# Kernel tuning notes

Hardware: AMD Instinct MI355X
Metric: run time of the kernel (lower is better)

Reference implementation:

```python
import jax, jax.numpy as jnp
import numpy as np

# ---- hyperparameters (from pars / init_kwargs) ----
ALPHA = 0.9          # synaptic conductance decay (snn.Synaptic alpha)
BETA = 0.8           # membrane decay (snn.Synaptic beta)
BETA_PLUS = 0.9      # pre-synaptic trace decay
BETA_MINUS = 0.9     # post-synaptic trace decay
THRESHOLD = 1.0
W_MIN, W_MAX = 0.0, 1.0
A_PLUS, A_MINUS = 0.008, 0.0008
T, B, IN, N = 350, 128, 784, 400
SPIKE_P = 0.05       # Bernoulli firing probability of the rate-coded input


def setup_inputs() -> dict:
    key = jax.random.key(0)
    k_img, k_w = jax.random.split(key)
    # Poisson/Bernoulli rate-coded MNIST spike train [T, B, IN]
    image = (jax.random.uniform(k_img, (T, B, IN)) < SPIKE_P).astype(jnp.float32)
    # nn.Linear default init U(-1/sqrt(IN), 1/sqrt(IN)) then clamp to [w_min, w_max]
    s = 1.0 / np.sqrt(IN)
    W = jnp.clip(jax.random.uniform(k_w, (N, IN), minval=-s, maxval=s), W_MIN, W_MAX)
    return {"image": image, "W": W}


def reference(image, W):
    """Fused LIF (snntorch Synaptic, reset-by-subtraction) + STDP loop over T steps.

    Returns (W_final, mem_final, syn_final, total_spikes_per_neuron).
    """
    batch = image.shape[1]

    def step(carry, x_t):
        syn, mem, pre_tr, post_tr, W = carry
        # pre-synaptic trace: tr_t = beta_plus * tr_{t-1} + x_t
        pre_tr = BETA_PLUS * pre_tr + x_t                      # [B, IN]
        # linear projection (no bias)
        I_t = jnp.einsum('bi,ni->bn', x_t, W)                  # [B, N]
        # snntorch Synaptic: reset from pre-update mem, subtract mechanism
        reset = (mem > THRESHOLD).astype(mem.dtype)
        syn = ALPHA * syn + I_t
        mem = BETA * mem + syn - reset * THRESHOLD
        spk = (mem > THRESHOLD).astype(mem.dtype)              # [B, N]
        # post-synaptic trace
        post_tr = BETA_MINUS * post_tr + spk
        # STDP: potentiate on post spike x pre trace, depress on pre spike x post trace
        dW = (A_PLUS * jnp.einsum('bn,bi->ni', spk, pre_tr)
              - A_MINUS * jnp.einsum('bn,bi->ni', post_tr, x_t)) / batch
        W = jnp.clip(W + dW, W_MIN, W_MAX)
        return (syn, mem, pre_tr, post_tr, W), spk.sum(axis=0)

    syn0 = jnp.zeros((batch, N), image.dtype)
    mem0 = jnp.zeros((batch, N), image.dtype)
    pre0 = jnp.zeros((batch, IN), image.dtype)
    post0 = jnp.zeros((batch, N), image.dtype)

    (syn, mem, _, _, W_final), spk_counts = jax.lax.scan(
        step, (syn0, mem0, pre0, post0, W), image)
    return W_final, mem, syn, spk_counts.sum(axis=0)
```

## Files before the change

kernel.cpp:

```cpp
#include <hip/hip_runtime.h>
#include <hip/hip_bf16.h>


#define TT    350
#define BB    128
#define INF   784
#define NNEU  400
#define NS    2
#define NTHR  1024
#define LCAP  80

#define ALPHA 0.9f
#define BETA  0.8f
#define BPLUS 0.9f
#define BMIN  0.9f
#define CP    (0.008f/128.0f)
#define CM    (0.0008f/128.0f)

__device__ __forceinline__ float bf2f(__hip_bfloat16 v){ return __bfloat162float(v); }

__device__ __forceinline__ void barx(){
  asm volatile("s_waitcnt lgkmcnt(0)" ::: "memory");
  __builtin_amdgcn_s_barrier();
  __builtin_amdgcn_sched_barrier(0);
}

__global__ void k_pretr(const float* __restrict__ img, __hip_bfloat16* __restrict__ pre){
  int idx = blockIdx.x*blockDim.x + threadIdx.x;
  if (idx >= BB*INF) return;
  float v = 0.f;
  for (int t=0;t<TT;t++){
    v = BPLUS*v + img[(size_t)t*(BB*INF) + idx];
    pre[(size_t)t*(BB*INF) + idx] = __float2bfloat16(v);
  }
}

__global__ void k_S(const __hip_bfloat16* __restrict__ pre, float* __restrict__ S){
  int idx = blockIdx.x*blockDim.x + threadIdx.x;
  if (idx >= TT*INF) return;
  int t = idx / INF, i = idx - t*INF;
  const __hip_bfloat16* p = pre + (size_t)t*(BB*INF) + i;
  float s = 0.f;
  for (int b=0;b<BB;b++) s += bf2f(p[(size_t)b*INF]);
  S[idx] = s;
}

__global__ void k_masks(const float* __restrict__ img,
                        unsigned short* __restrict__ lists,
                        int* __restrict__ cnts,
                        unsigned int* __restrict__ collist){
  __shared__ unsigned long long rowbits[BB][13];
  __shared__ unsigned short buf[16][LCAP];
  const int t = blockIdx.x;
  const int tid = threadIdx.x, lane = tid & 63, w = tid >> 6;
  const float* base = img + (size_t)t*(BB*INF);

  for (int r8=0; r8<8; r8++){
    int r = w*8 + r8;
    const float* p = base + (size_t)r*INF;
    for (int c=0;c<13;c++){
      int i = c*64 + lane;
      bool a = (i < INF) && (p[i] > 0.f);
      unsigned long long bal = __ballot(a);
      if (lane == 0) rowbits[r][c] = bal;
    }
  }
  for (int r8=0; r8<8; r8++){
    int r = w*8 + r8;
    int cnt = 0;
    for (int c=0;c<13;c++){
      unsigned long long word = rowbits[r][c];
      int i = c*64 + lane;
      bool a = (word >> lane) & 1ull;
      int pos = cnt + __popcll(word & ((1ull<<lane)-1ull));
      if (a && pos < LCAP) buf[w][pos] = (unsigned short)(i<<3);
      cnt += __popcll(word);
    }
    for (int k = cnt + lane; k < LCAP; k += 64) buf[w][k] = (unsigned short)(INF<<3);
    if (lane == 0) cnts[t*BB + r] = (cnt < LCAP) ? cnt : LCAP;
    if (lane < LCAP/2)
      ((unsigned int*)(lists + (size_t)(t*BB + r)*LCAP))[lane] = ((unsigned int*)buf[w])[lane];
  }
  __syncthreads();
  if (tid < INF){
    int wsel = tid >> 6, bit = tid & 63;
    unsigned long long m0=0, m1=0;
    for (int b=0;b<64;b++) m0 |= ((rowbits[b][wsel]    >> bit) & 1ull) << b;
    for (int b=0;b<64;b++) m1 |= ((rowbits[64+b][wsel] >> bit) & 1ull) << b;
    int cnt = __popcll(m0) + __popcll(m1);
    unsigned int wd[8];
    wd[0] = (unsigned int)cnt; wd[1]=0;wd[2]=0;wd[3]=0;wd[4]=0;wd[5]=0;wd[6]=0;wd[7]=0;
    #pragma unroll
    for (int k=1;k<32;k++){
      int bb;
      if (m0){ bb = __builtin_ctzll(m0); m0 &= m0-1; }
      else if (m1){ bb = 64 + __builtin_ctzll(m1); m1 &= m1-1; }
      else bb = 128;
      wd[k>>2] |= ((unsigned int)bb) << ((k&3)*8);
    }
    uint4* dst = (uint4*)(collist + ((size_t)t*INF + tid)*8);
    uint4 lo; lo.x=wd[0]; lo.y=wd[1]; lo.z=wd[2]; lo.w=wd[3];
    uint4 hi; hi.x=wd[4]; hi.y=wd[5]; hi.z=wd[6]; hi.w=wd[7];
    dst[0]=lo; dst[1]=hi;
  }
}

__device__ __forceinline__ float potf(unsigned long long ma, unsigned long long mb,
                                      int pc, float Sv,
                                      const __hip_bfloat16* __restrict__ prt, int c){
  bool direct = (pc <= 64);
  unsigned long long m = direct ? ma : ~ma;
  unsigned long long n = direct ? mb : ~mb;
  float acc = 0.f;
  while (m){ int bb = __builtin_ctzll(m); m &= m-1; acc += bf2f(prt[(size_t)bb*INF + c]); }
  while (n){ int bb = __builtin_ctzll(n); n &= n-1; acc += bf2f(prt[(size_t)(64+bb)*INF + c]); }
  return direct ? acc : (Sv - acc);
}

#define G2(W) { float2 a_ = *(const float2*)((const char*)&Wp2[0] + ((W) & 0xffffu)); I0 += a_.x; I1 += a_.y; \
                float2 b_ = *(const float2*)((const char*)&Wp2[0] + ((W) >> 16));     I0 += b_.x; I1 += b_.y; }
#define GATHER8(V) { G2((V).x); G2((V).y); G2((V).z); G2((V).w); }

#define DEP4(W) { float2 p_; \
  p_ = postl[(W) & 0xffu];        d0 += p_.x; d1 += p_.y; \
  p_ = postl[((W)>>8) & 0xffu];   d0 += p_.x; d1 += p_.y; \
  p_ = postl[((W)>>16) & 0xffu];  d0 += p_.x; d1 += p_.y; \
  p_ = postl[(W)>>24];            d0 += p_.x; d1 += p_.y; }

#define DOCOL(c, cl, sv) { \
  float d0=0.f, d1=0.f; \
  unsigned int w0_ = (cl).x; \
  { float2 p_; \
    p_ = postl[(w0_>>8) & 0xffu];  d0 += p_.x; d1 += p_.y; \
    p_ = postl[(w0_>>16) & 0xffu]; d0 += p_.x; d1 += p_.y; \
    p_ = postl[w0_>>24];           d0 += p_.x; d1 += p_.y; } \
  DEP4((cl).y); DEP4((cl).z); DEP4((cl).w); \
  int cc_ = (int)(w0_ & 0xffu); \
  if (cc_ > 15){ \
    uint4 e2_ = *(const uint4*)(collist + ((size_t)t*INF + (c))*8 + 4); \
    DEP4(e2_.x); DEP4(e2_.y); DEP4(e2_.z); DEP4(e2_.w); \
  } \
  float pot0_ = potf(s00, s01, pc0, (sv), prt, (c)); \
  float pot1_ = potf(s10, s11, pc1, (sv), prt, (c)); \
  float2 wv_ = Wp2[(c)]; \
  wv_.x = fminf(fmaxf(wv_.x + CP*pot0_ - CM*d0, 0.f), 1.f); \
  wv_.y = fminf(fmaxf(wv_.y + CP*pot1_ - CM*d1, 0.f), 1.f); \
  Wp2[(c)] = wv_; }

__launch_bounds__(NTHR, 1)
__global__ void k_main(const float* __restrict__ Win,
                       const __hip_bfloat16* __restrict__ pre,
                       const float* __restrict__ S,
                       const unsigned short* __restrict__ lists,
                       const int* __restrict__ cnts,
                       const unsigned int* __restrict__ collist,
                       float* __restrict__ out){
  __shared__ float2 Wp2[800];
  __shared__ float2 postl[132];
  __shared__ unsigned long long smQ[2][2];
  __shared__ float cntS[2];
  __shared__ float2 postCb[2];
  __shared__ int    unifb[2];

  const int tid  = threadIdx.x;
  const int lane = tid & 63;
  const int wv   = tid >> 6;
  const int q    = lane >> 3;
  const int b    = (wv << 3) | (lane & 7);
  const int n0   = blockIdx.x * NS;

  if (tid < 800){
    float2 w;
    w.x = (tid < INF) ? Win[(size_t)n0*INF + tid] : 0.f;
    w.y = (tid < INF) ? Win[(size_t)(n0+1)*INF + tid] : 0.f;
    Wp2[tid] = w;
  }
  if (tid < 132){ postl[tid].x = 0.f; postl[tid].y = 0.f; }
  if (tid < 2) cntS[tid] = 0.f;
  if (tid == 0){
    postCb[0].x = 0.f; postCb[0].y = 0.f; unifb[0] = 1;
    postCb[1].x = 0.f; postCb[1].y = 0.f; unifb[1] = 1;
  }

  const int  c0   = tid;
  const bool hasc = (c0 < INF);

  float syn0=0.f, mem0=0.f, syn1=0.f, mem1=0.f, sc0=0.f, sc1=0.f;

  uint4 lA = *(const uint4*)(lists + ((size_t)b)*LCAP + (size_t)q*8);
  int cn = cnts[b];
  uint4 cl0; cl0.x=0;cl0.y=0;cl0.z=0;cl0.w=0;
  float sv0 = 0.f;
  if (hasc){ cl0 = *(const uint4*)(collist + (size_t)c0*8); sv0 = S[c0]; }

  __syncthreads();

  for (int t=0; t<TT; t++){
    float I0 = 0.f, I1 = 0.f;
    GATHER8(lA);
    if (cn > 64 + q*8){
      uint4 lC = *(const uint4*)(lists + ((size_t)t*BB + b)*LCAP + 64 + (size_t)q*8);
      GATHER8(lC);
    }
    int tn = (t+1 < TT) ? t+1 : TT-1;
    uint4 lAn = *(const uint4*)(lists + ((size_t)tn*BB + b)*LCAP + (size_t)q*8);
    int cnn = cnts[tn*BB + b];
    uint4 cl0n = cl0; float sv0n = sv0;
    if (hasc){
      cl0n = *(const uint4*)(collist + ((size_t)tn*INF + c0)*8);
      sv0n = S[tn*INF + c0];
    }

    I0 += __shfl_xor(I0, 8); I0 += __shfl_xor(I0, 16); I0 += __shfl_xor(I0, 32);
    I1 += __shfl_xor(I1, 8); I1 += __shfl_xor(I1, 16); I1 += __shfl_xor(I1, 32);

    float r0 = (mem0 > 1.f) ? 1.f : 0.f;
    syn0 = ALPHA*syn0 + I0;
    mem0 = BETA*mem0 + syn0 - r0;
    float s0 = (mem0 > 1.f) ? 1.f : 0.f;
    float r1 = (mem1 > 1.f) ? 1.f : 0.f;
    syn1 = ALPHA*syn1 + I1;
    mem1 = BETA*mem1 + syn1 - r1;
    float s1 = (mem1 > 1.f) ? 1.f : 0.f;
    unsigned long long bal0 = __ballot(s0 > 0.5f);
    unsigned long long bal1 = __ballot(s1 > 0.5f);
    if (q == 0){
      sc0 += s0; sc1 += s1;
      float2 pv = postl[b];
      pv.x = BMIN*pv.x + s0;
      pv.y = BMIN*pv.y + s1;
      postl[b] = pv;
    }
    if (lane == 0){
      ((unsigned char*)smQ)[wv]      = (unsigned char)(bal0 & 0xffu);
      ((unsigned char*)smQ)[16 + wv] = (unsigned char)(bal1 & 0xffu);
    }
    barx();

    unsigned long long s00 = smQ[0][0], s01 = smQ[0][1];
    unsigned long long s10 = smQ[1][0], s11 = smQ[1][1];
    bool full0 = (s00 & s01) == ~0ull, none0 = (s00 | s01) == 0ull;
    bool full1 = (s10 & s11) == ~0ull, none1 = (s10 | s11) == 0ull;
    int   fastOK = unifb[t & 1] && (full0 || none0) && (full1 || none1);
    float2 pC = postCb[t & 1];

    if (wv == 13){
      float2 a0 = postl[lane], a1 = postl[64 + lane];
      float2 rr = postl[0];
      bool eq = (a0.x==rr.x) && (a0.y==rr.y) && (a1.x==rr.x) && (a1.y==rr.y);
      unsigned long long bal = __ballot(eq);
      if (lane == 0){ unifb[(t+1) & 1] = (bal == ~0ull); postCb[(t+1) & 1] = rr; }
    }

    if (fastOK){
      if (hasc){
        float sa0 = full0 ? 1.f : 0.f, sa1 = full1 ? 1.f : 0.f;
        float cur0 = BMIN*pC.x + sa0, cur1 = BMIN*pC.y + sa1;
        bool allzero = none0 && none1 && (pC.x == 0.f) && (pC.y == 0.f);
        if (!allzero){
          float cc  = (float)(int)(cl0.x & 0xffu);
          float pot0 = full0 ? sv0 : 0.f;
          float pot1 = full1 ? sv0 : 0.f;
          float2 wv_ = Wp2[c0];
          wv_.x = fminf(fmaxf(wv_.x + CP*pot0 - CM*(cur0*cc), 0.f), 1.f);
          wv_.y = fminf(fmaxf(wv_.y + CP*pot1 - CM*(cur1*cc), 0.f), 1.f);
          Wp2[c0] = wv_;
        }
      }
    } else {
      int pc0 = __popcll(s00) + __popcll(s01);
      int pc1 = __popcll(s10) + __popcll(s11);
      const __hip_bfloat16* prt = pre + (size_t)t*(BB*INF);
      if (hasc) DOCOL(c0, cl0, sv0)
    }

    lA=lAn; cn=cnn; cl0=cl0n; sv0=sv0n;
    barx();
  }

  __syncthreads();
  if (tid < INF){
    float2 wvv = Wp2[tid];
    out[(size_t)n0*INF + tid]       = wvv.x;
    out[(size_t)(n0+1)*INF + tid]   = wvv.y;
  }
  if (q == 0){
    out[(size_t)NNEU*INF + (size_t)b*NNEU + n0]                        = mem0;
    out[(size_t)NNEU*INF + (size_t)b*NNEU + n0 + 1]                    = mem1;
    out[(size_t)NNEU*INF + (size_t)BB*NNEU + (size_t)b*NNEU + n0]      = syn0;
    out[(size_t)NNEU*INF + (size_t)BB*NNEU + (size_t)b*NNEU + n0 + 1]  = syn1;
    atomicAdd(&cntS[0], sc0);
    atomicAdd(&cntS[1], sc1);
  }
  __syncthreads();
  if (tid < 2) out[(size_t)NNEU*INF + 2*(size_t)BB*NNEU + n0 + tid] = cntS[tid];
}

extern "C" void kernel_launch(void* const* d_in, const int* in_sizes, int n_in,
                              void* d_out, int out_size, void* d_ws, size_t ws_size,
                              hipStream_t stream) {
  const float* img = (const float*)d_in[0];
  const float* W   = (const float*)d_in[1];
  float* out = (float*)d_out;

  char* ws = (char*)d_ws;
  __hip_bfloat16* pre  = (__hip_bfloat16*)ws;
  float*          S    = (float*)(ws + 70246400);
  unsigned short* lst  = (unsigned short*)(ws + 71344000);
  int*            cnts = (int*)(ws + 78512000);
  unsigned int*   coll = (unsigned int*)(ws + 78691200);

  k_pretr<<<(BB*INF + 255)/256, 256, 0, stream>>>(img, pre);
  k_masks<<<TT, NTHR, 0, stream>>>(img, lst, cnts, coll);
  k_S    <<<(TT*INF + 255)/256, 256, 0, stream>>>(pre, S);
  k_main <<<NNEU/NS, NTHR, 0, stream>>>(W, pre, S, lst, cnts, coll, out);
}
```

Baseline: 727.5 us.

## Compute potentiation incrementally from spike-mask deltas and drop column-sum precompute kernel

Potentiation term sum_b spk[b]*pre_tr[b,i] is now carried across timesteps: the trace recurrence gives BPLUS*previous + popcount(column mask & previous spikes), and only batches whose spike state flipped need a gather from the pre-trace buffer. This replaces the per-step mask walk and the uniform-spike fast path, and removes the k_S column-sum kernel. k_masks additionally stores raw 128-bit column masks. The batch-to-lane mapping is changed so the I reduction uses DPP row operations instead of cross-lane shuffles. The risks are float drift from the recursive accumulation compared with the bf16-based gathers, and the added per-column mask traffic.

```diff
diff --git a/kernel.cpp b/kernel.cpp
--- a/kernel.cpp
+++ b/kernel.cpp
@@ -25,6 +25,13 @@
   __builtin_amdgcn_sched_barrier(0);
 }
 
+__device__ __forceinline__ float dppred(float x){
+  x += __int_as_float(__builtin_amdgcn_update_dpp(0, __float_as_int(x), 0x4E,  0xF, 0xF, true));
+  x += __int_as_float(__builtin_amdgcn_update_dpp(0, __float_as_int(x), 0x124, 0xF, 0xF, true));
+  x += __int_as_float(__builtin_amdgcn_update_dpp(0, __float_as_int(x), 0x128, 0xF, 0xF, true));
+  return x;
+}
+
 __global__ void k_pretr(const float* __restrict__ img, __hip_bfloat16* __restrict__ pre){
   int idx = blockIdx.x*blockDim.x + threadIdx.x;
   if (idx >= BB*INF) return;
@@ -35,20 +42,11 @@
   }
 }
 
-__global__ void k_S(const __hip_bfloat16* __restrict__ pre, float* __restrict__ S){
-  int idx = blockIdx.x*blockDim.x + threadIdx.x;
-  if (idx >= TT*INF) return;
-  int t = idx / INF, i = idx - t*INF;
-  const __hip_bfloat16* p = pre + (size_t)t*(BB*INF) + i;
-  float s = 0.f;
-  for (int b=0;b<BB;b++) s += bf2f(p[(size_t)b*INF]);
-  S[idx] = s;
-}
-
 __global__ void k_masks(const float* __restrict__ img,
                         unsigned short* __restrict__ lists,
                         int* __restrict__ cnts,
-                        unsigned int* __restrict__ collist){
+                        unsigned int* __restrict__ collist,
+                        ulonglong2* __restrict__ rawcm){
   __shared__ unsigned long long rowbits[BB][13];
   __shared__ unsigned short buf[16][LCAP];
   const int t = blockIdx.x;
@@ -87,6 +85,8 @@
     unsigned long long m0=0, m1=0;
     for (int b=0;b<64;b++) m0 |= ((rowbits[b][wsel]    >> bit) & 1ull) << b;
     for (int b=0;b<64;b++) m1 |= ((rowbits[64+b][wsel] >> bit) & 1ull) << b;
+    ulonglong2 rm; rm.x = m0; rm.y = m1;
+    rawcm[(size_t)t*INF + tid] = rm;
     int cnt = __popcll(m0) + __popcll(m1);
     unsigned int wd[8];
     wd[0] = (unsigned int)cnt; wd[1]=0;wd[2]=0;wd[3]=0;wd[4]=0;wd[5]=0;wd[6]=0;wd[7]=0;
@@ -105,18 +105,6 @@
   }
 }
 
-__device__ __forceinline__ float potf(unsigned long long ma, unsigned long long mb,
-                                      int pc, float Sv,
-                                      const __hip_bfloat16* __restrict__ prt, int c){
-  bool direct = (pc <= 64);
-  unsigned long long m = direct ? ma : ~ma;
-  unsigned long long n = direct ? mb : ~mb;
-  float acc = 0.f;
-  while (m){ int bb = __builtin_ctzll(m); m &= m-1; acc += bf2f(prt[(size_t)bb*INF + c]); }
-  while (n){ int bb = __builtin_ctzll(n); n &= n-1; acc += bf2f(prt[(size_t)(64+bb)*INF + c]); }
-  return direct ? acc : (Sv - acc);
-}
-
 #define G2(W) { float2 a_ = *(const float2*)((const char*)&Wp2[0] + ((W) & 0xffffu)); I0 += a_.x; I1 += a_.y; \
                 float2 b_ = *(const float2*)((const char*)&Wp2[0] + ((W) >> 16));     I0 += b_.x; I1 += b_.y; }
 #define GATHER8(V) { G2((V).x); G2((V).y); G2((V).z); G2((V).w); }
@@ -127,46 +115,24 @@
   p_ = postl[((W)>>16) & 0xffu];  d0 += p_.x; d1 += p_.y; \
   p_ = postl[(W)>>24];            d0 += p_.x; d1 += p_.y; }
 
-#define DOCOL(c, cl, sv) { \
-  float d0=0.f, d1=0.f; \
-  unsigned int w0_ = (cl).x; \
-  { float2 p_; \
-    p_ = postl[(w0_>>8) & 0xffu];  d0 += p_.x; d1 += p_.y; \
-    p_ = postl[(w0_>>16) & 0xffu]; d0 += p_.x; d1 += p_.y; \
-    p_ = postl[w0_>>24];           d0 += p_.x; d1 += p_.y; } \
-  DEP4((cl).y); DEP4((cl).z); DEP4((cl).w); \
-  int cc_ = (int)(w0_ & 0xffu); \
-  if (cc_ > 15){ \
-    uint4 e2_ = *(const uint4*)(collist + ((size_t)t*INF + (c))*8 + 4); \
-    DEP4(e2_.x); DEP4(e2_.y); DEP4(e2_.z); DEP4(e2_.w); \
-  } \
-  float pot0_ = potf(s00, s01, pc0, (sv), prt, (c)); \
-  float pot1_ = potf(s10, s11, pc1, (sv), prt, (c)); \
-  float2 wv_ = Wp2[(c)]; \
-  wv_.x = fminf(fmaxf(wv_.x + CP*pot0_ - CM*d0, 0.f), 1.f); \
-  wv_.y = fminf(fmaxf(wv_.y + CP*pot1_ - CM*d1, 0.f), 1.f); \
-  Wp2[(c)] = wv_; }
-
 __launch_bounds__(NTHR, 1)
 __global__ void k_main(const float* __restrict__ Win,
                        const __hip_bfloat16* __restrict__ pre,
-                       const float* __restrict__ S,
                        const unsigned short* __restrict__ lists,
                        const int* __restrict__ cnts,
                        const unsigned int* __restrict__ collist,
+                       const ulonglong2* __restrict__ rawcm,
                        float* __restrict__ out){
   __shared__ float2 Wp2[800];
   __shared__ float2 postl[132];
   __shared__ unsigned long long smQ[2][2];
   __shared__ float cntS[2];
-  __shared__ float2 postCb[2];
-  __shared__ int    unifb[2];
 
   const int tid  = threadIdx.x;
   const int lane = tid & 63;
   const int wv   = tid >> 6;
-  const int q    = lane >> 3;
-  const int b    = (wv << 3) | (lane & 7);
+  const int q    = (lane >> 1) & 7;
+  const int b    = (lane & 1) | (((lane >> 4) & 3) << 1) | (wv << 3);
   const int n0   = blockIdx.x * NS;
 
   if (tid < 800){
@@ -177,21 +143,20 @@
   }
   if (tid < 132){ postl[tid].x = 0.f; postl[tid].y = 0.f; }
   if (tid < 2) cntS[tid] = 0.f;
-  if (tid == 0){
-    postCb[0].x = 0.f; postCb[0].y = 0.f; unifb[0] = 1;
-    postCb[1].x = 0.f; postCb[1].y = 0.f; unifb[1] = 1;
-  }
 
   const int  c0   = tid;
   const bool hasc = (c0 < INF);
 
   float syn0=0.f, mem0=0.f, syn1=0.f, mem1=0.f, sc0=0.f, sc1=0.f;
+  float potR0=0.f, potR1=0.f;
+  unsigned long long p00=0ull, p01=0ull, p10=0ull, p11=0ull;
+  bool anyEver = false;
 
   uint4 lA = *(const uint4*)(lists + ((size_t)b)*LCAP + (size_t)q*8);
   int cn = cnts[b];
   uint4 cl0; cl0.x=0;cl0.y=0;cl0.z=0;cl0.w=0;
-  float sv0 = 0.f;
-  if (hasc){ cl0 = *(const uint4*)(collist + (size_t)c0*8); sv0 = S[c0]; }
+  ulonglong2 cm0; cm0.x=0; cm0.y=0;
+  if (hasc){ cl0 = *(const uint4*)(collist + (size_t)c0*8); cm0 = rawcm[c0]; }
 
   __syncthreads();
 
@@ -205,14 +170,14 @@
     int tn = (t+1 < TT) ? t+1 : TT-1;
     uint4 lAn = *(const uint4*)(lists + ((size_t)tn*BB + b)*LCAP + (size_t)q*8);
     int cnn = cnts[tn*BB + b];
-    uint4 cl0n = cl0; float sv0n = sv0;
+    uint4 cl0n = cl0; ulonglong2 cm0n = cm0;
     if (hasc){
       cl0n = *(const uint4*)(collist + ((size_t)tn*INF + c0)*8);
-      sv0n = S[tn*INF + c0];
-    }
-
-    I0 += __shfl_xor(I0, 8); I0 += __shfl_xor(I0, 16); I0 += __shfl_xor(I0, 32);
-    I1 += __shfl_xor(I1, 8); I1 += __shfl_xor(I1, 16); I1 += __shfl_xor(I1, 32);
+      cm0n = rawcm[(size_t)tn*INF + c0];
+    }
+
+    I0 = dppred(I0);
+    I1 = dppred(I1);
 
     float r0 = (mem0 > 1.f) ? 1.f : 0.f;
     syn0 = ALPHA*syn0 + I0;
@@ -232,49 +197,58 @@
       postl[b] = pv;
     }
     if (lane == 0){
-      ((unsigned char*)smQ)[wv]      = (unsigned char)(bal0 & 0xffu);
-      ((unsigned char*)smQ)[16 + wv] = (unsigned char)(bal1 & 0xffu);
+      unsigned int by0 = (unsigned int)((bal0 & 3ull) | ((bal0>>16)&3ull)<<2 |
+                                        ((bal0>>32)&3ull)<<4 | ((bal0>>48)&3ull)<<6);
+      unsigned int by1 = (unsigned int)((bal1 & 3ull) | ((bal1>>16)&3ull)<<2 |
+                                        ((bal1>>32)&3ull)<<4 | ((bal1>>48)&3ull)<<6);
+      ((unsigned char*)smQ)[wv]      = (unsigned char)by0;
+      ((unsigned char*)smQ)[16 + wv] = (unsigned char)by1;
     }
     barx();
 
     unsigned long long s00 = smQ[0][0], s01 = smQ[0][1];
     unsigned long long s10 = smQ[1][0], s11 = smQ[1][1];
-    bool full0 = (s00 & s01) == ~0ull, none0 = (s00 | s01) == 0ull;
-    bool full1 = (s10 & s11) == ~0ull, none1 = (s10 | s11) == 0ull;
-    int   fastOK = unifb[t & 1] && (full0 || none0) && (full1 || none1);
-    float2 pC = postCb[t & 1];
-
-    if (wv == 13){
-      float2 a0 = postl[lane], a1 = postl[64 + lane];
-      float2 rr = postl[0];
-      bool eq = (a0.x==rr.x) && (a0.y==rr.y) && (a1.x==rr.x) && (a1.y==rr.y);
-      unsigned long long bal = __ballot(eq);
-      if (lane == 0){ unifb[(t+1) & 1] = (bal == ~0ull); postCb[(t+1) & 1] = rr; }
-    }
-
-    if (fastOK){
-      if (hasc){
-        float sa0 = full0 ? 1.f : 0.f, sa1 = full1 ? 1.f : 0.f;
-        float cur0 = BMIN*pC.x + sa0, cur1 = BMIN*pC.y + sa1;
-        bool allzero = none0 && none1 && (pC.x == 0.f) && (pC.y == 0.f);
-        if (!allzero){
-          float cc  = (float)(int)(cl0.x & 0xffu);
-          float pot0 = full0 ? sv0 : 0.f;
-          float pot1 = full1 ? sv0 : 0.f;
-          float2 wv_ = Wp2[c0];
-          wv_.x = fminf(fmaxf(wv_.x + CP*pot0 - CM*(cur0*cc), 0.f), 1.f);
-          wv_.y = fminf(fmaxf(wv_.y + CP*pot1 - CM*(cur1*cc), 0.f), 1.f);
-          Wp2[c0] = wv_;
-        }
+    bool anyNow = ((s00|s01|s10|s11) != 0ull);
+    bool runD = anyEver || anyNow;
+    anyEver = runD;
+
+    if (runD && hasc){
+      float d0=0.f, d1=0.f;
+      unsigned int w0_ = cl0.x;
+      { float2 p_;
+        p_ = postl[(w0_>>8) & 0xffu];  d0 += p_.x; d1 += p_.y;
+        p_ = postl[(w0_>>16) & 0xffu]; d0 += p_.x; d1 += p_.y;
+        p_ = postl[w0_>>24];           d0 += p_.x; d1 += p_.y; }
+      DEP4(cl0.y); DEP4(cl0.z); DEP4(cl0.w);
+      int cc_ = (int)(w0_ & 0xffu);
+      if (cc_ > 15){
+        uint4 e2_ = *(const uint4*)(collist + ((size_t)t*INF + c0)*8 + 4);
+        DEP4(e2_.x); DEP4(e2_.y); DEP4(e2_.z); DEP4(e2_.w);
       }
-    } else {
-      int pc0 = __popcll(s00) + __popcll(s01);
-      int pc1 = __popcll(s10) + __popcll(s11);
-      const __hip_bfloat16* prt = pre + (size_t)t*(BB*INF);
-      if (hasc) DOCOL(c0, cl0, sv0)
-    }
-
-    lA=lAn; cn=cnn; cl0=cl0n; sv0=sv0n;
+      float pot0 = BPLUS*potR0 + (float)(__popcll(cm0.x & p00) + __popcll(cm0.y & p01));
+      float pot1 = BPLUS*potR1 + (float)(__popcll(cm0.x & p10) + __popcll(cm0.y & p11));
+      unsigned long long f00 = (s00^p00) & cm0.x, f01 = (s01^p01) & cm0.y;
+      unsigned long long f10 = (s10^p10) & cm0.x, f11 = (s11^p11) & cm0.y;
+      if (f00|f01|f10|f11){
+        const __hip_bfloat16* prow = pre + (size_t)t*(BB*INF) + c0;
+        while (f00){ int bb=__builtin_ctzll(f00); f00&=f00-1;
+          float v=bf2f(prow[(size_t)bb*INF]);      pot0 += ((s00>>bb)&1ull)? v : -v; }
+        while (f01){ int bb=__builtin_ctzll(f01); f01&=f01-1;
+          float v=bf2f(prow[(size_t)(64+bb)*INF]); pot0 += ((s01>>bb)&1ull)? v : -v; }
+        while (f10){ int bb=__builtin_ctzll(f10); f10&=f10-1;
+          float v=bf2f(prow[(size_t)bb*INF]);      pot1 += ((s10>>bb)&1ull)? v : -v; }
+        while (f11){ int bb=__builtin_ctzll(f11); f11&=f11-1;
+          float v=bf2f(prow[(size_t)(64+bb)*INF]); pot1 += ((s11>>bb)&1ull)? v : -v; }
+      }
+      potR0 = pot0; potR1 = pot1;
+      float2 wv_ = Wp2[c0];
+      wv_.x = fminf(fmaxf(wv_.x + CP*pot0 - CM*d0, 0.f), 1.f);
+      wv_.y = fminf(fmaxf(wv_.y + CP*pot1 - CM*d1, 0.f), 1.f);
+      Wp2[c0] = wv_;
+    }
+    p00=s00; p01=s01; p10=s10; p11=s11;
+
+    lA=lAn; cn=cnn; cl0=cl0n; cm0=cm0n;
     barx();
   }
 
@@ -305,13 +279,12 @@
 
   char* ws = (char*)d_ws;
   __hip_bfloat16* pre  = (__hip_bfloat16*)ws;
-  float*          S    = (float*)(ws + 70246400);
-  unsigned short* lst  = (unsigned short*)(ws + 71344000);
-  int*            cnts = (int*)(ws + 78512000);
-  unsigned int*   coll = (unsigned int*)(ws + 78691200);
+  unsigned short* lst  = (unsigned short*)(ws + 70246400);
+  int*            cnts = (int*)(ws + 77414400);
+  unsigned int*   coll = (unsigned int*)(ws + 77593600);
+  ulonglong2*     rcm  = (ulonglong2*)(ws + 86374400);
 
   k_pretr<<<(BB*INF + 255)/256, 256, 0, stream>>>(img, pre);
-  k_masks<<<TT, NTHR, 0, stream>>>(img, lst, cnts, coll);
-  k_S    <<<(TT*INF + 255)/256, 256, 0, stream>>>(pre, S);
-  k_main <<<NNEU/NS, NTHR, 0, stream>>>(W, pre, S, lst, cnts, coll, out);
-}
+  k_masks<<<TT, NTHR, 0, stream>>>(img, lst, cnts, coll, rcm);
+  k_main <<<NNEU/NS, NTHR, 0, stream>>>(W, pre, lst, cnts, coll, rcm, out);
+}
```

Measured after the change: 785.0 us. 1.08x slower.
